# Kernel optimization log

Measured on AMD Instinct MI355X. Metric: run time of the kernel, lower is better.

The kernel has to match this reference:

```python
import jax, jax.numpy as jnp
import numpy as np
from jax import lax

C_IN, C_OUT, H, W = 64, 128, 512, 512


def setup_inputs() -> dict:
    key = jax.random.key(0)
    k1, k2, k3, k4 = jax.random.split(key, 4)
    x = jax.random.normal(k1, (C_IN, H, W), dtype=jnp.float32)
    # Conv2d params (eqx default: kernel 3x3, bias used). Small init scale for stability.
    conv_w = jax.random.normal(k2, (C_OUT, C_IN, 3, 3), dtype=jnp.float32) * 0.05
    conv_b = jax.random.normal(k3, (C_OUT,), dtype=jnp.float32) * 0.05
    fft_mask = jax.random.normal(k4, (C_OUT, H, W), dtype=jnp.float32)
    return {"x": x, "conv_w": conv_w, "conv_b": conv_b, "fft_mask": fft_mask}


def reference(x, conv_w, conv_b, fft_mask):
    # 3x3 same-padding conv on a single (C,H,W) sample -> (C_OUT,H,W)
    y = lax.conv_general_dilated(
        x[None],  # (1,C_IN,H,W)
        conv_w,
        window_strides=(1, 1),
        padding=((1, 1), (1, 1)),
        dimension_numbers=("NCHW", "OIHW", "NCHW"),
    )[0] + conv_b[:, None, None]
    # Per-channel spectral filter: FFT over (H,W), elementwise complex-mask
    # multiply, inverse FFT, take real part. Vectorized over channels.
    Y = jnp.fft.fftn(y, axes=(1, 2)) * fft_mask
    return jnp.fft.ifftn(Y, axes=(1, 2)).real
```

## Files before the change

### kernel.cpp

```cpp
#include <hip/hip_runtime.h>

#define CIN   64
#define COUT  128
#define HH    512
#define WW    512
#define HW    (HH*WW)

typedef __attribute__((ext_vector_type(8))) short  short8;
typedef __attribute__((ext_vector_type(4))) float  floatx4;


__device__ __forceinline__ unsigned short f2bf(float f) {
    unsigned u = __float_as_uint(f);
    u += 0x7fffu + ((u >> 16) & 1u);
    return (unsigned short)(u >> 16);
}


__global__ __launch_bounds__(256) void k_wprep(
        const float* __restrict__ cw,
        unsigned short* __restrict__ wt)
{
    int i = blockIdx.x * 256 + threadIdx.x;
    int tap = i >> 13;
    int co  = (i >> 6) & 127;
    int ci  = i & 63;
    wt[i] = f2bf(cw[(co * 64 + ci) * 9 + tap]);
}


__global__ __launch_bounds__(256) void k_xprep(
        const float* __restrict__ x,
        unsigned short* __restrict__ xt)
{
    __shared__ unsigned short tile[64][72];
    int t  = threadIdx.x;
    int h  = blockIdx.x >> 3;
    int w0 = (blockIdx.x & 7) << 6;
    int wl = t & 63;
#pragma unroll
    for (int it = 0; it < 16; ++it) {
        int ci = (t >> 6) + 4 * it;
        tile[wl][ci] = f2bf(x[ci * HW + h * 512 + w0 + wl]);
    }
    __syncthreads();
#pragma unroll
    for (int it = 0; it < 2; ++it) {
        int task = t + 256 * it;
        int w = task >> 3, seg = task & 7;
        *(short8*)&xt[((size_t)(h * 512 + w0 + w)) * 64 + seg * 8] =
            *(const short8*)&tile[w][seg * 8];
    }
}


__global__ __launch_bounds__(256) void k_maskT2(
        const float* __restrict__ mask,
        float* __restrict__ mt)
{
    __shared__ float t1[64][65];
    __shared__ float t2[64][65];
    int b  = blockIdx.x;
    int ch = b >> 6;
    int k0 = ((b >> 3) & 7) << 6;
    int c0 = (b & 7) << 6;
    int t  = threadIdx.x;
    int j  = t & 63, i0 = t >> 6;
    const float* mch = mask + (size_t)ch * HW;
#pragma unroll
    for (int it = 0; it < 16; ++it) {
        int i  = i0 + 4 * it;
        int mi = (512 - (k0 + i)) & 511;
        int mj = (512 - (c0 + j)) & 511;
        t1[i][j] = mch[(size_t)(k0 + i) * 512 + (c0 + j)];
        t2[i][j] = mch[(size_t)mi * 512 + mj];
    }
    __syncthreads();
    float* och = mt + (size_t)ch * HW;
#pragma unroll
    for (int it = 0; it < 16; ++it) {
        int jj = i0 + 4 * it;
        och[(size_t)(c0 + jj) * 512 + k0 + j] = t1[j][jj] + t2[j][jj];
    }
}


__global__ __launch_bounds__(512) void k_conv(
        const unsigned short* __restrict__ xt,
        const unsigned short* __restrict__ wt,
        const float* __restrict__ bias,
        float* __restrict__ y)
{
    __shared__ __align__(16) unsigned short As[3][130][68];

    int b  = blockIdx.x;
    int h  = b >> 2;
    int w0 = (b & 3) << 7;
    int t  = threadIdx.x;
    int lane = t & 63, wv = t >> 6;
    int wm = wv >> 2, wn = wv & 3;
    int l15 = lane & 15, quad = lane >> 4;

    for (int idx = t; idx < 3 * 130 * 8; idx += 512) {
        int dy  = idx / 1040;
        int rem = idx - dy * 1040;
        int p   = rem >> 3, seg = rem & 7;
        int hp  = h + dy - 1;
        int wq  = w0 - 1 + p;
        short8 v = {0, 0, 0, 0, 0, 0, 0, 0};
        if ((unsigned)hp < 512u && (unsigned)wq < 512u)
            v = *(const short8*)&xt[((size_t)(hp * 512 + wq)) * 64 + seg * 8];
        *(short8*)&As[dy][p][seg * 8] = v;
    }
    __syncthreads();

    floatx4 acc[4][2];
#pragma unroll
    for (int mt = 0; mt < 4; ++mt)
#pragma unroll
        for (int nt = 0; nt < 2; ++nt) {
            floatx4 z = {0.f, 0.f, 0.f, 0.f};
            acc[mt][nt] = z;
        }

#pragma unroll
    for (int tap = 0; tap < 9; ++tap) {
        int dy = tap / 3, dx = tap - dy * 3;
        short8 bfr[2][2];
#pragma unroll
        for (int nt = 0; nt < 2; ++nt)
#pragma unroll
            for (int kc = 0; kc < 2; ++kc) {
                int co = wn * 32 + nt * 16 + l15;
                bfr[nt][kc] = *(const short8*)
                    &wt[(tap * 128 + co) * 64 + kc * 32 + quad * 8];
            }
#pragma unroll
        for (int kc = 0; kc < 2; ++kc) {
            int c0 = kc * 32 + quad * 8;
            short8 afr[4];
#pragma unroll
            for (int mt = 0; mt < 4; ++mt) {
                int row = wm * 64 + mt * 16 + l15 + dx;
                afr[mt] = *(const short8*)&As[dy][row][c0];
            }
#pragma unroll
            for (int mt = 0; mt < 4; ++mt)
#pragma unroll
                for (int nt = 0; nt < 2; ++nt)
                    acc[mt][nt] = __builtin_amdgcn_mfma_f32_16x16x32_bf16(
                        afr[mt], bfr[nt][kc], acc[mt][nt], 0, 0, 0);
        }
    }

#pragma unroll
    for (int nt = 0; nt < 2; ++nt) {
        int co = wn * 32 + nt * 16 + l15;
        float bv = bias[co];
#pragma unroll
        for (int mt = 0; mt < 4; ++mt) {
            floatx4 o = acc[mt][nt];
            o[0] += bv; o[1] += bv; o[2] += bv; o[3] += bv;
            int m = wm * 64 + mt * 16 + quad * 4;
            *(floatx4*)&y[co * HW + h * 512 + w0 + m] = o;
        }
    }
}


#define FS 576

template<int MODE>
__device__ __forceinline__ int slotf(int c, int a) {
    return (MODE == 0) ? c * FS + ((a + (a >> 3)) ^ c)
                       : a * 16 + (c ^ (a & 15));
}

__device__ __forceinline__ float2 cadd(float2 a, float2 b){ return make_float2(a.x+b.x, a.y+b.y); }
__device__ __forceinline__ float2 csub(float2 a, float2 b){ return make_float2(a.x-b.x, a.y-b.y); }

template<int DIR> __device__ __forceinline__ float2 twmul(float2 a, float2 t){
    return (DIR > 0) ? make_float2(a.x*t.x - a.y*t.y, a.x*t.y + a.y*t.x)
                     : make_float2(a.x*t.x + a.y*t.y, a.y*t.x - a.x*t.y);
}
template<int DIR> __device__ __forceinline__ float2 mulJ(float2 a){
    return (DIR > 0) ? make_float2(a.y, -a.x) : make_float2(-a.y, a.x);
}

#define RSQRT2 0.70710678118654752f

template<int DIR> __device__ __forceinline__ void dft8(float2* x){
    float2 a0 = cadd(x[0], x[4]), b0 = csub(x[0], x[4]);
    float2 a1 = cadd(x[1], x[5]), b1 = csub(x[1], x[5]);
    float2 a2 = cadd(x[2], x[6]), b2 = csub(x[2], x[6]);
    float2 a3 = cadd(x[3], x[7]), b3 = csub(x[3], x[7]);
    b1 = (DIR > 0) ? make_float2((b1.x + b1.y)*RSQRT2, (b1.y - b1.x)*RSQRT2)
                   : make_float2((b1.x - b1.y)*RSQRT2, (b1.y + b1.x)*RSQRT2);
    b2 = mulJ<DIR>(b2);
    b3 = (DIR > 0) ? make_float2((b3.y - b3.x)*RSQRT2, -(b3.x + b3.y)*RSQRT2)
                   : make_float2(-(b3.x + b3.y)*RSQRT2, (b3.x - b3.y)*RSQRT2);
    float2 c0 = cadd(a0, a2), d0 = csub(a0, a2);
    float2 c1 = cadd(a1, a3), d1 = mulJ<DIR>(csub(a1, a3));
    x[0] = cadd(c0, c1); x[4] = csub(c0, c1);
    x[2] = cadd(d0, d1); x[6] = csub(d0, d1);
    float2 e0 = cadd(b0, b2), f0 = csub(b0, b2);
    float2 e1 = cadd(b1, b3), f1 = mulJ<DIR>(csub(b1, b3));
    x[1] = cadd(e0, e1); x[5] = csub(e0, e1);
    x[3] = cadd(f0, f1); x[7] = csub(f0, f1);
}

template<int MODE>
__device__ __forceinline__ void fft512_fwd(float2 X[4][8], float2* buf,
                                           const float2* tw, int w, int c) {
#pragma unroll
    for (int b = 0; b < 4; ++b) {
        dft8<1>(X[b]);
        int g = w + 16*b;
#pragma unroll
        for (int k = 1; k < 8; ++k) X[b][k] = twmul<1>(X[b][k], tw[g*k]);
    }
#pragma unroll
    for (int b = 0; b < 4; ++b) {
        int g = w + 16*b;
#pragma unroll
        for (int k = 0; k < 8; ++k) buf[slotf<MODE>(c, k*64 + g)] = X[b][k];
    }
    __syncthreads();
#pragma unroll
    for (int b = 0; b < 4; ++b) {
        int u = w + 16*b; int bs = (u >> 3)*64 + (u & 7);
#pragma unroll
        for (int g2 = 0; g2 < 8; ++g2) X[b][g2] = buf[slotf<MODE>(c, bs + 8*g2)];
    }
#pragma unroll
    for (int b = 0; b < 4; ++b) {
        dft8<1>(X[b]);
        int g1 = (w + 16*b) & 7;
#pragma unroll
        for (int k = 1; k < 8; ++k) X[b][k] = twmul<1>(X[b][k], tw[8*g1*k]);
    }
    __syncthreads();
#pragma unroll
    for (int b = 0; b < 4; ++b) {
        int u = w + 16*b; int bs = (u >> 3)*64 + (u & 7);
#pragma unroll
        for (int k = 0; k < 8; ++k) buf[slotf<MODE>(c, bs + 8*k)] = X[b][k];
    }
    __syncthreads();
#pragma unroll
    for (int b = 0; b < 4; ++b) {
        int v = w + 16*b;
#pragma unroll
        for (int g1 = 0; g1 < 8; ++g1) X[b][g1] = buf[slotf<MODE>(c, 8*v + g1)];
    }
#pragma unroll
    for (int b = 0; b < 4; ++b) dft8<1>(X[b]);
}

template<int MODE>
__device__ __forceinline__ void fft512_inv(float2 X[4][8], float2* buf,
                                           const float2* tw, int w, int c) {
#pragma unroll
    for (int b = 0; b < 4; ++b) dft8<-1>(X[b]);
    __syncthreads();
#pragma unroll
    for (int b = 0; b < 4; ++b) {
        int v = w + 16*b;
#pragma unroll
        for (int g1 = 0; g1 < 8; ++g1) buf[slotf<MODE>(c, 8*v + g1)] = X[b][g1];
    }
    __syncthreads();
#pragma unroll
    for (int b = 0; b < 4; ++b) {
        int u = w + 16*b; int bs = (u >> 3)*64 + (u & 7);
#pragma unroll
        for (int k = 0; k < 8; ++k) X[b][k] = buf[slotf<MODE>(c, bs + 8*k)];
    }
#pragma unroll
    for (int b = 0; b < 4; ++b) {
        int g1 = (w + 16*b) & 7;
#pragma unroll
        for (int k = 1; k < 8; ++k) X[b][k] = twmul<-1>(X[b][k], tw[8*g1*k]);
        dft8<-1>(X[b]);
    }
    __syncthreads();
#pragma unroll
    for (int b = 0; b < 4; ++b) {
        int u = w + 16*b; int bs = (u >> 3)*64 + (u & 7);
#pragma unroll
        for (int g2 = 0; g2 < 8; ++g2) buf[slotf<MODE>(c, bs + 8*g2)] = X[b][g2];
    }
    __syncthreads();
#pragma unroll
    for (int b = 0; b < 4; ++b) {
        int g = w + 16*b;
#pragma unroll
        for (int k = 0; k < 8; ++k) X[b][k] = buf[slotf<MODE>(c, k*64 + g)];
    }
#pragma unroll
    for (int b = 0; b < 4; ++b) {
        int g = w + 16*b;
#pragma unroll
        for (int k = 1; k < 8; ++k) X[b][k] = twmul<-1>(X[b][k], tw[g*k]);
        dft8<-1>(X[b]);
    }
}

__device__ __forceinline__ void build_tw(float2* tw, int t) {
    const float a0 = -6.283185307179586f / 512.0f;
    float s, c;
    __sincosf(a0 * (float)t, &s, &c);         tw[t]       = make_float2(c, s);
    __sincosf(a0 * (float)(t + 256), &s, &c); tw[t + 256] = make_float2(c, s);
}


__global__ __launch_bounds__(256) void k_rows_fwd_pair(
        const float* __restrict__ y,
        float2* __restrict__ Z)
{
    __shared__ float2 buf[16 * FS];
    __shared__ float2 tw[512];
    int t = threadIdx.x;
    build_tw(tw, t);
    int c = t >> 4, w = t & 15;
    int p = blockIdx.x >> 5, r0 = (blockIdx.x & 31) << 4;
    const float* yA = y + (size_t)(2*p) * HW;
    const float* yB = yA + HW;

    for (int it = 0; it < 16; ++it) {
        int n = t + 256*it;
        int rr = n >> 8, q = n & 255;
        float2 a2 = *(const float2*)&yA[(size_t)(r0 + rr)*512 + 2*q];
        float2 b2 = *(const float2*)&yB[(size_t)(r0 + rr)*512 + 2*q];
        buf[slotf<0>(rr, 2*q)]     = make_float2(a2.x, b2.x);
        buf[slotf<0>(rr, 2*q + 1)] = make_float2(a2.y, b2.y);
    }
    __syncthreads();
    float2 X[4][8];
#pragma unroll
    for (int b = 0; b < 4; ++b)
#pragma unroll
        for (int r = 0; r < 8; ++r)
            X[b][r] = buf[slotf<0>(c, w + 16*b + 64*r)];
    __syncthreads();
    fft512_fwd<0>(X, buf, tw, w, c);

    __syncthreads();
#pragma unroll
    for (int b = 0; b < 4; ++b) {
        int v = w + 16*b; int kb = (v >> 3) + 8*(v & 7);
#pragma unroll
        for (int m = 0; m < 8; ++m) buf[slotf<0>(c, kb + 64*m)] = X[b][m];
    }
    __syncthreads();
    size_t zb = (size_t)p * HW + r0;
    for (int it = 0; it < 32; ++it) {
        int n = t + 256*it;
        int col = n >> 4, rr = n & 15;
        Z[zb + (size_t)col*512 + rr] = buf[slotf<0>(rr, col)];
    }
}

__device__ __forceinline__ int col_of(int g, int j) {
    if (g == 0) return (j < 8) ? j : (j == 8 ? 256 : 496 + j);
    return (j < 8) ? 8*g + j : 512 - 8*g - 15 + j;
}
__device__ __forceinline__ int jmir(int g, int j) {
    return (g == 0) ? ((16 - j) & 15) : (15 - j);
}

__global__ __launch_bounds__(256) void k_cols_pair(
        float2* __restrict__ Z,
        const float* __restrict__ mt)
{
    __shared__ float2 buf[8192];
    __shared__ float2 tw[512];
    int t = threadIdx.x;
    build_tw(tw, t);
    int c = t & 15, w = t >> 4;
    int p = blockIdx.x >> 5, g = blockIdx.x & 31;
    int colc = col_of(g, c);
    int cm   = jmir(g, c);
    size_t zch = (size_t)p * HW;
    const float* mAp = mt + (size_t)(2*p) * HW + (size_t)colc * 512;
    const float* mBp = mAp + HW;

    for (int it = 0; it < 32; ++it) {
        int n = t + 256*it;
        int cj = n >> 9, row = n & 511;
        buf[slotf<1>(cj, row)] = Z[zch + (size_t)col_of(g, cj)*512 + row];
    }
    float Sa[4][8], Sb[4][8];
#pragma unroll
    for (int b = 0; b < 4; ++b) {
        int v = w + 16*b; int kb = (v >> 3) + 8*(v & 7);
#pragma unroll
        for (int m = 0; m < 8; ++m) {
            int k1 = kb + 64*m;
            Sa[b][m] = mAp[k1];
            Sb[b][m] = mBp[k1];
        }
    }
    __syncthreads();
    float2 X[4][8];
#pragma unroll
    for (int b = 0; b < 4; ++b)
#pragma unroll
        for (int r = 0; r < 8; ++r)
            X[b][r] = buf[slotf<1>(c, w + 16*b + 64*r)];
    __syncthreads();
    fft512_fwd<1>(X, buf, tw, w, c);

    __syncthreads();
#pragma unroll
    for (int b = 0; b < 4; ++b) {
        int v = w + 16*b; int kb = (v >> 3) + 8*(v & 7);
#pragma unroll
        for (int m = 0; m < 8; ++m) buf[slotf<1>(c, kb + 64*m)] = X[b][m];
    }
    __syncthreads();

    const float s4 = 0.25f / 262144.0f;
#pragma unroll
    for (int b = 0; b < 4; ++b) {
        int v = w + 16*b; int kb = (v >> 3) + 8*(v & 7);
#pragma unroll
        for (int m = 0; m < 8; ++m) {
            int k1  = kb + 64*m;
            int mk1 = (512 - k1) & 511;
            float2 P = X[b][m];
            float2 Q = buf[slotf<1>(cm, mk1)];
            float alpha = (Sa[b][m] + Sb[b][m]) * s4;
            float beta  = (Sa[b][m] - Sb[b][m]) * s4;
            X[b][m] = make_float2(alpha * P.x + beta * Q.x,
                                  alpha * P.y - beta * Q.y);
        }
    }
    fft512_inv<1>(X, buf, tw, w, c);
    __syncthreads();
#pragma unroll
    for (int b = 0; b < 4; ++b)
#pragma unroll
        for (int r = 0; r < 8; ++r)
            buf[slotf<1>(c, w + 16*b + 64*r)] = X[b][r];
    __syncthreads();
    for (int it = 0; it < 32; ++it) {
        int n = t + 256*it;
        int cj = n >> 9, row = n & 511;
        Z[zch + (size_t)col_of(g, cj)*512 + row] = buf[slotf<1>(cj, row)];
    }
}

__global__ __launch_bounds__(256) void k_rows_inv_pair(
        const float2* __restrict__ Z,
        float* __restrict__ out)
{
    __shared__ float2 buf[16 * FS];
    __shared__ float2 tw[512];
    int t = threadIdx.x;
    build_tw(tw, t);
    int c = t >> 4, w = t & 15;
    int p = blockIdx.x >> 5, r0 = (blockIdx.x & 31) << 4;
    size_t zb = (size_t)p * HW + r0;

    for (int it = 0; it < 32; ++it) {
        int n = t + 256*it;
        int col = n >> 4, rr = n & 15;
        buf[slotf<0>(rr, col)] = Z[zb + (size_t)col*512 + rr];
    }
    __syncthreads();

    float2 X[4][8];
#pragma unroll
    for (int b = 0; b < 4; ++b) {
        int v = w + 16*b; int kb = (v >> 3) + 8*(v & 7);
#pragma unroll
        for (int m = 0; m < 8; ++m) X[b][m] = buf[slotf<0>(c, kb + 64*m)];
    }
    fft512_inv<0>(X, buf, tw, w, c);
    __syncthreads();
#pragma unroll
    for (int b = 0; b < 4; ++b)
#pragma unroll
        for (int r = 0; r < 8; ++r)
            buf[slotf<0>(c, w + 16*b + 64*r)] = X[b][r];
    __syncthreads();
    float* oA = out + (size_t)(2*p) * HW;
    float* oB = oA + HW;
    for (int it = 0; it < 16; ++it) {
        int n = t + 256*it;
        int rr = n >> 8, q = n & 255;
        float2 v0 = buf[slotf<0>(rr, 2*q)];
        float2 v1 = buf[slotf<0>(rr, 2*q + 1)];
        *(float2*)&oA[(size_t)(r0 + rr)*512 + 2*q] = make_float2(v0.x, v1.x);
        *(float2*)&oB[(size_t)(r0 + rr)*512 + 2*q] = make_float2(v0.y, v1.y);
    }
}


extern "C" void kernel_launch(void* const* d_in, const int* in_sizes, int n_in,
                              void* d_out, int out_size, void* d_ws, size_t ws_size,
                              hipStream_t stream) {
    const float* x    = (const float*)d_in[0];
    const float* cw   = (const float*)d_in[1];
    const float* cb   = (const float*)d_in[2];
    const float* mask = (const float*)d_in[3];

    float*  outRe = (float*)d_out;
    float2* ZT    = (float2*)d_ws;

    unsigned short* xt = (unsigned short*)d_ws;
    unsigned short* wt = (unsigned short*)d_ws + (size_t)HW * 64;

    k_wprep<<<288, 256, 0, stream>>>(cw, wt);
    k_xprep<<<4096, 256, 0, stream>>>(x, xt);
    k_conv<<<2048, 512, 0, stream>>>(xt, wt, cb, outRe);
    k_rows_fwd_pair<<<2048, 256, 0, stream>>>(outRe, ZT);
    k_maskT2<<<8192, 256, 0, stream>>>(mask, outRe);
    k_cols_pair<<<2048, 256, 0, stream>>>(ZT, outRe);
    k_rows_inv_pair<<<2048, 256, 0, stream>>>(ZT, outRe);
}
```

Before: 652.8 us.

## Replace block barriers inside 512-point FFTs with wavefront-local syncs

Every FFT is now owned by a group of 16 threads (c = t>>4), so all 16 threads of one transform sit in the same 64-wide wavefront. The column kernel's thread mapping and shared-memory layout are switched to the row-style padded layout to allow this. The block-wide __syncthreads inside the FFT stages are then replaced by a wave barrier plus an LDS wait. This removes many workgroup barriers per FFT, but correctness now depends on the wave-local data ownership holding for every shared-memory exchange.

```diff
diff --git a/kernel.cpp b/kernel.cpp
--- a/kernel.cpp
+++ b/kernel.cpp
@@ -14,6 +14,15 @@
     unsigned u = __float_as_uint(f);
     u += 0x7fffu + ((u >> 16) & 1u);
     return (unsigned short)(u >> 16);
+}
+
+__device__ __forceinline__ void wave_sync() {
+    __builtin_amdgcn_wave_barrier();
+    asm volatile("s_waitcnt lgkmcnt(0)" ::: "memory");
+    __builtin_amdgcn_sched_barrier(0);
+}
+template<bool BLK> __device__ __forceinline__ void xsync() {
+    if (BLK) __syncthreads(); else wave_sync();
 }
 
 
@@ -170,10 +179,8 @@
 
 #define FS 576
 
-template<int MODE>
 __device__ __forceinline__ int slotf(int c, int a) {
-    return (MODE == 0) ? c * FS + ((a + (a >> 3)) ^ c)
-                       : a * 16 + (c ^ (a & 15));
+    return c * FS + ((a + (a >> 3)) ^ c);
 }
 
 __device__ __forceinline__ float2 cadd(float2 a, float2 b){ return make_float2(a.x+b.x, a.y+b.y); }
@@ -209,7 +216,7 @@
     x[3] = cadd(f0, f1); x[7] = csub(f0, f1);
 }
 
-template<int MODE>
+template<bool BLK>
 __device__ __forceinline__ void fft512_fwd(float2 X[4][8], float2* buf,
                                            const float2* tw, int w, int c) {
 #pragma unroll
@@ -223,14 +230,14 @@
     for (int b = 0; b < 4; ++b) {
         int g = w + 16*b;
 #pragma unroll
-        for (int k = 0; k < 8; ++k) buf[slotf<MODE>(c, k*64 + g)] = X[b][k];
-    }
-    __syncthreads();
+        for (int k = 0; k < 8; ++k) buf[slotf(c, k*64 + g)] = X[b][k];
+    }
+    xsync<BLK>();
 #pragma unroll
     for (int b = 0; b < 4; ++b) {
         int u = w + 16*b; int bs = (u >> 3)*64 + (u & 7);
 #pragma unroll
-        for (int g2 = 0; g2 < 8; ++g2) X[b][g2] = buf[slotf<MODE>(c, bs + 8*g2)];
+        for (int g2 = 0; g2 < 8; ++g2) X[b][g2] = buf[slotf(c, bs + 8*g2)];
     }
 #pragma unroll
     for (int b = 0; b < 4; ++b) {
@@ -239,42 +246,42 @@
 #pragma unroll
         for (int k = 1; k < 8; ++k) X[b][k] = twmul<1>(X[b][k], tw[8*g1*k]);
     }
-    __syncthreads();
+    xsync<BLK>();
 #pragma unroll
     for (int b = 0; b < 4; ++b) {
         int u = w + 16*b; int bs = (u >> 3)*64 + (u & 7);
 #pragma unroll
-        for (int k = 0; k < 8; ++k) buf[slotf<MODE>(c, bs + 8*k)] = X[b][k];
-    }
-    __syncthreads();
+        for (int k = 0; k < 8; ++k) buf[slotf(c, bs + 8*k)] = X[b][k];
+    }
+    xsync<BLK>();
 #pragma unroll
     for (int b = 0; b < 4; ++b) {
         int v = w + 16*b;
 #pragma unroll
-        for (int g1 = 0; g1 < 8; ++g1) X[b][g1] = buf[slotf<MODE>(c, 8*v + g1)];
+        for (int g1 = 0; g1 < 8; ++g1) X[b][g1] = buf[slotf(c, 8*v + g1)];
     }
 #pragma unroll
     for (int b = 0; b < 4; ++b) dft8<1>(X[b]);
 }
 
-template<int MODE>
+template<bool BLK>
 __device__ __forceinline__ void fft512_inv(float2 X[4][8], float2* buf,
                                            const float2* tw, int w, int c) {
 #pragma unroll
     for (int b = 0; b < 4; ++b) dft8<-1>(X[b]);
-    __syncthreads();
+    xsync<BLK>();
 #pragma unroll
     for (int b = 0; b < 4; ++b) {
         int v = w + 16*b;
 #pragma unroll
-        for (int g1 = 0; g1 < 8; ++g1) buf[slotf<MODE>(c, 8*v + g1)] = X[b][g1];
-    }
-    __syncthreads();
+        for (int g1 = 0; g1 < 8; ++g1) buf[slotf(c, 8*v + g1)] = X[b][g1];
+    }
+    xsync<BLK>();
 #pragma unroll
     for (int b = 0; b < 4; ++b) {
         int u = w + 16*b; int bs = (u >> 3)*64 + (u & 7);
 #pragma unroll
-        for (int k = 0; k < 8; ++k) X[b][k] = buf[slotf<MODE>(c, bs + 8*k)];
+        for (int k = 0; k < 8; ++k) X[b][k] = buf[slotf(c, bs + 8*k)];
     }
 #pragma unroll
     for (int b = 0; b < 4; ++b) {
@@ -283,19 +290,19 @@
         for (int k = 1; k < 8; ++k) X[b][k] = twmul<-1>(X[b][k], tw[8*g1*k]);
         dft8<-1>(X[b]);
     }
-    __syncthreads();
+    xsync<BLK>();
 #pragma unroll
     for (int b = 0; b < 4; ++b) {
         int u = w + 16*b; int bs = (u >> 3)*64 + (u & 7);
 #pragma unroll
-        for (int g2 = 0; g2 < 8; ++g2) buf[slotf<MODE>(c, bs + 8*g2)] = X[b][g2];
-    }
-    __syncthreads();
+        for (int g2 = 0; g2 < 8; ++g2) buf[slotf(c, bs + 8*g2)] = X[b][g2];
+    }
+    xsync<BLK>();
 #pragma unroll
     for (int b = 0; b < 4; ++b) {
         int g = w + 16*b;
 #pragma unroll
-        for (int k = 0; k < 8; ++k) X[b][k] = buf[slotf<MODE>(c, k*64 + g)];
+        for (int k = 0; k < 8; ++k) X[b][k] = buf[slotf(c, k*64 + g)];
     }
 #pragma unroll
     for (int b = 0; b < 4; ++b) {
@@ -332,8 +339,8 @@
         int rr = n >> 8, q = n & 255;
         float2 a2 = *(const float2*)&yA[(size_t)(r0 + rr)*512 + 2*q];
         float2 b2 = *(const float2*)&yB[(size_t)(r0 + rr)*512 + 2*q];
-        buf[slotf<0>(rr, 2*q)]     = make_float2(a2.x, b2.x);
-        buf[slotf<0>(rr, 2*q + 1)] = make_float2(a2.y, b2.y);
+        buf[slotf(rr, 2*q)]     = make_float2(a2.x, b2.x);
+        buf[slotf(rr, 2*q + 1)] = make_float2(a2.y, b2.y);
     }
     __syncthreads();
     float2 X[4][8];
@@ -341,23 +348,23 @@
     for (int b = 0; b < 4; ++b)
 #pragma unroll
         for (int r = 0; r < 8; ++r)
-            X[b][r] = buf[slotf<0>(c, w + 16*b + 64*r)];
-    __syncthreads();
-    fft512_fwd<0>(X, buf, tw, w, c);
-
-    __syncthreads();
+            X[b][r] = buf[slotf(c, w + 16*b + 64*r)];
+    wave_sync();
+    fft512_fwd<false>(X, buf, tw, w, c);
+
+    wave_sync();
 #pragma unroll
     for (int b = 0; b < 4; ++b) {
         int v = w + 16*b; int kb = (v >> 3) + 8*(v & 7);
 #pragma unroll
-        for (int m = 0; m < 8; ++m) buf[slotf<0>(c, kb + 64*m)] = X[b][m];
+        for (int m = 0; m < 8; ++m) buf[slotf(c, kb + 64*m)] = X[b][m];
     }
     __syncthreads();
     size_t zb = (size_t)p * HW + r0;
     for (int it = 0; it < 32; ++it) {
         int n = t + 256*it;
         int col = n >> 4, rr = n & 15;
-        Z[zb + (size_t)col*512 + rr] = buf[slotf<0>(rr, col)];
+        Z[zb + (size_t)col*512 + rr] = buf[slotf(rr, col)];
     }
 }
 
@@ -373,11 +380,11 @@
         float2* __restrict__ Z,
         const float* __restrict__ mt)
 {
-    __shared__ float2 buf[8192];
+    __shared__ float2 buf[16 * FS];
     __shared__ float2 tw[512];
     int t = threadIdx.x;
     build_tw(tw, t);
-    int c = t & 15, w = t >> 4;
+    int c = t >> 4, w = t & 15;
     int p = blockIdx.x >> 5, g = blockIdx.x & 31;
     int colc = col_of(g, c);
     int cm   = jmir(g, c);
@@ -388,7 +395,7 @@
     for (int it = 0; it < 32; ++it) {
         int n = t + 256*it;
         int cj = n >> 9, row = n & 511;
-        buf[slotf<1>(cj, row)] = Z[zch + (size_t)col_of(g, cj)*512 + row];
+        buf[slotf(cj, row)] = Z[zch + (size_t)col_of(g, cj)*512 + row];
     }
     float Sa[4][8], Sb[4][8];
 #pragma unroll
@@ -407,16 +414,16 @@
     for (int b = 0; b < 4; ++b)
 #pragma unroll
         for (int r = 0; r < 8; ++r)
-            X[b][r] = buf[slotf<1>(c, w + 16*b + 64*r)];
-    __syncthreads();
-    fft512_fwd<1>(X, buf, tw, w, c);
-
-    __syncthreads();
+            X[b][r] = buf[slotf(c, w + 16*b + 64*r)];
+    wave_sync();
+    fft512_fwd<false>(X, buf, tw, w, c);
+
+    wave_sync();
 #pragma unroll
     for (int b = 0; b < 4; ++b) {
         int v = w + 16*b; int kb = (v >> 3) + 8*(v & 7);
 #pragma unroll
-        for (int m = 0; m < 8; ++m) buf[slotf<1>(c, kb + 64*m)] = X[b][m];
+        for (int m = 0; m < 8; ++m) buf[slotf(c, kb + 64*m)] = X[b][m];
     }
     __syncthreads();
 
@@ -429,25 +436,26 @@
             int k1  = kb + 64*m;
             int mk1 = (512 - k1) & 511;
             float2 P = X[b][m];
-            float2 Q = buf[slotf<1>(cm, mk1)];
+            float2 Q = buf[slotf(cm, mk1)];
             float alpha = (Sa[b][m] + Sb[b][m]) * s4;
             float beta  = (Sa[b][m] - Sb[b][m]) * s4;
             X[b][m] = make_float2(alpha * P.x + beta * Q.x,
                                   alpha * P.y - beta * Q.y);
         }
     }
-    fft512_inv<1>(X, buf, tw, w, c);
-    __syncthreads();
+    __syncthreads();
+    fft512_inv<false>(X, buf, tw, w, c);
+    wave_sync();
 #pragma unroll
     for (int b = 0; b < 4; ++b)
 #pragma unroll
         for (int r = 0; r < 8; ++r)
-            buf[slotf<1>(c, w + 16*b + 64*r)] = X[b][r];
+            buf[slotf(c, w + 16*b + 64*r)] = X[b][r];
     __syncthreads();
     for (int it = 0; it < 32; ++it) {
         int n = t + 256*it;
         int cj = n >> 9, row = n & 511;
-        Z[zch + (size_t)col_of(g, cj)*512 + row] = buf[slotf<1>(cj, row)];
+        Z[zch + (size_t)col_of(g, cj)*512 + row] = buf[slotf(cj, row)];
     }
 }
 
@@ -466,7 +474,7 @@
     for (int it = 0; it < 32; ++it) {
         int n = t + 256*it;
         int col = n >> 4, rr = n & 15;
-        buf[slotf<0>(rr, col)] = Z[zb + (size_t)col*512 + rr];
+        buf[slotf(rr, col)] = Z[zb + (size_t)col*512 + rr];
     }
     __syncthreads();
 
@@ -475,23 +483,23 @@
     for (int b = 0; b < 4; ++b) {
         int v = w + 16*b; int kb = (v >> 3) + 8*(v & 7);
 #pragma unroll
-        for (int m = 0; m < 8; ++m) X[b][m] = buf[slotf<0>(c, kb + 64*m)];
-    }
-    fft512_inv<0>(X, buf, tw, w, c);
-    __syncthreads();
+        for (int m = 0; m < 8; ++m) X[b][m] = buf[slotf(c, kb + 64*m)];
+    }
+    fft512_inv<false>(X, buf, tw, w, c);
+    wave_sync();
 #pragma unroll
     for (int b = 0; b < 4; ++b)
 #pragma unroll
         for (int r = 0; r < 8; ++r)
-            buf[slotf<0>(c, w + 16*b + 64*r)] = X[b][r];
+            buf[slotf(c, w + 16*b + 64*r)] = X[b][r];
     __syncthreads();
     float* oA = out + (size_t)(2*p) * HW;
     float* oB = oA + HW;
     for (int it = 0; it < 16; ++it) {
         int n = t + 256*it;
         int rr = n >> 8, q = n & 255;
-        float2 v0 = buf[slotf<0>(rr, 2*q)];
-        float2 v1 = buf[slotf<0>(rr, 2*q + 1)];
+        float2 v0 = buf[slotf(rr, 2*q)];
+        float2 v1 = buf[slotf(rr, 2*q + 1)];
         *(float2*)&oA[(size_t)(r0 + rr)*512 + 2*q] = make_float2(v0.x, v1.x);
         *(float2*)&oB[(size_t)(r0 + rr)*512 + 2*q] = make_float2(v0.y, v1.y);
     }
```

Measured after the change: 631.1 us. 3.3% less time.
